# Kernel optimization log

Hardware: AMD Instinct MI355X
Metric: run time of the kernel (lower is better)

## Reference

```python
import jax, jax.numpy as jnp
import numpy as np
import math

EPS = 1e-6
NUM_HEADS = 8


def _layernorm(x, g, b):
    mu = jnp.mean(x, axis=-1, keepdims=True)
    var = jnp.mean(jnp.square(x - mu), axis=-1, keepdims=True)
    return (x - mu) * jax.lax.rsqrt(var + EPS) * g + b


def _pos_embed(n, d):
    pos = jnp.arange(n, dtype=jnp.float32)[:, None]                  # [N,1]
    div = jnp.exp(jnp.arange(0, d, 2, dtype=jnp.float32) * (-math.log(10000.0) / d))
    ang = pos * div                                                  # [N,d/2]
    pe = jnp.stack([jnp.sin(ang), jnp.cos(ang)], axis=-1).reshape(n, d)
    return pe


def setup_inputs() -> dict:
    key = jax.random.key(0)
    B, N, C, L = 2, 2048, 256, 4
    ks = jax.random.split(key, 6)
    s = 0.02
    return {
        "x": jax.random.normal(ks[0], (B, N, C), jnp.float32),
        "qkv_w": jax.random.normal(ks[1], (L, C, 3 * C), jnp.float32) * s,
        "proj_w": jax.random.normal(ks[2], (L, C, C), jnp.float32) * s,
        "proj_b": jnp.zeros((L, C), jnp.float32),
        "w1": jax.random.normal(ks[3], (L, C, C), jnp.float32) * s,
        "b1": jnp.zeros((L, C), jnp.float32),
        "w2": jax.random.normal(ks[4], (L, C, C), jnp.float32) * s,
        "b2": jnp.zeros((L, C), jnp.float32),
        "g1": jnp.ones((L, C), jnp.float32),
        "be1": jnp.zeros((L, C), jnp.float32),
        "g2": jnp.ones((L, C), jnp.float32),
        "be2": jnp.zeros((L, C), jnp.float32),
    }


def reference(x, qkv_w, proj_w, proj_b, w1, b1, w2, b2, g1, be1, g2, be2):
    B, N, C = x.shape
    L = qkv_w.shape[0]
    H = NUM_HEADS
    dh = C // H
    scale = dh ** -0.5

    x = x + _pos_embed(N, C)[None]

    for l in range(L):
        # --- attention (manual QKV, post-norm residual as in source) ---
        qkv = (x @ qkv_w[l]).reshape(B, N, 3, H, dh)
        q, k, v = qkv[:, :, 0], qkv[:, :, 1], qkv[:, :, 2]           # [B,N,H,dh]
        attn = jnp.einsum('bqhd,bkhd->bhqk', q, k) * scale           # [B,H,N,N]
        attn = jax.nn.softmax(attn, axis=-1)
        o = jnp.einsum('bhqk,bkhd->bqhd', attn, v).reshape(B, N, C)
        o = o @ proj_w[l] + proj_b[l]
        x = _layernorm(x + o, g1[l], be1[l])
        # --- MLP (GELU exact, as torch nn.GELU default) ---
        m = jax.nn.gelu(x @ w1[l] + b1[l], approximate=False) @ w2[l] + b2[l]
        x = _layernorm(x + m, g2[l], be2[l])
    return x
```

## Files before the change

kernel.cpp:

```cpp
#include <hip/hip_runtime.h>
#include <math.h>

#define Bd 2
#define Nd 2048
#define Cd 256
#define Ld 4
#define Hd 8
#define Md (Bd*Nd)
#define BHd 16
#define U32d 1024
#define SPLITd 4

typedef __attribute__((ext_vector_type(8))) short bf16x8;
typedef __attribute__((ext_vector_type(4))) float f32x4;
typedef __attribute__((ext_vector_type(16))) float f32x16;
typedef __attribute__((ext_vector_type(4))) short shortx4;

static __device__ inline f32x4 mfma16(bf16x8 a, bf16x8 b, f32x4 c) {
    return __builtin_amdgcn_mfma_f32_16x16x32_bf16(a, b, c, 0, 0, 0);
}
static __device__ inline f32x16 mfma32(bf16x8 a, bf16x8 b, f32x16 c) {
    return __builtin_amdgcn_mfma_f32_32x32x16_bf16(a, b, c, 0, 0, 0);
}
static __device__ inline short f2bf(float f) {
    union { float f; unsigned u; } v; v.f = f;
    unsigned r = (v.u + 0x7fff + ((v.u >> 16) & 1)) >> 16;
    return (short)r;
}
static __device__ inline unsigned pkbf(float a, float b) {
    unsigned r;
    asm("v_cvt_pk_bf16_f32 %0, %1, %2" : "=v"(r) : "v"(a), "v"(b));
    return r;
}
static __device__ inline float bf2f(unsigned u) {
    return __uint_as_float((u & 0xffffu) << 16);
}

__global__ __launch_bounds__(256)
void prep_kernel(const float* __restrict__ x_in, const float* __restrict__ qkv_w,
                 const float* __restrict__ proj_w, const float* __restrict__ w1,
                 const float* __restrict__ w2, float* __restrict__ xf,
                 short* __restrict__ xb, short* __restrict__ qkvT,
                 short* __restrict__ projT, short* __restrict__ w1T,
                 short* __restrict__ w2T, float qscale)
{
    __shared__ float tile[32][33];
    int id = blockIdx.x;
    if (id < 1536) {
        const float* src; short* dst; int Nc; float scale; int lim; int rem; int l;
        if (id < 768)       { l = id / 192;         rem = id % 192; src = qkv_w;  dst = qkvT;  Nc = 768; scale = qscale; lim = 256; }
        else if (id < 1024) { l = (id - 768) / 64;  rem = (id - 768) % 64;  src = proj_w; dst = projT; Nc = 256; scale = 1.f; lim = 0; }
        else if (id < 1280) { l = (id - 1024) / 64; rem = (id - 1024) % 64; src = w1;     dst = w1T;   Nc = 256; scale = 1.f; lim = 0; }
        else                { l = (id - 1280) / 64; rem = (id - 1280) % 64; src = w2;     dst = w2T;   Nc = 256; scale = 1.f; lim = 0; }
        int nb = Nc >> 5;
        int c0 = (rem % nb) * 32, k0 = (rem / nb) * 32;
        src += (size_t)l * 256 * Nc;
        dst += (size_t)l * Nc * 256;
        int tx = threadIdx.x & 31, ty = threadIdx.x >> 5;
#pragma unroll
        for (int i = 0; i < 4; i++) {
            int k = ty + 8 * i;
            tile[k][tx] = src[(size_t)(k0 + k) * Nc + c0 + tx];
        }
        __syncthreads();
#pragma unroll
        for (int i = 0; i < 4; i++) {
            int cc = ty + 8 * i;
            int col = c0 + cc;
            float v = tile[tx][cc];
            if (col < lim) v *= scale;
            dst[(size_t)col * 256 + k0 + tx] = f2bf(v);
        }
    } else {
        int i = (id - 1536) * 256 + threadIdx.x;
        int c = i & (Cd - 1);
        int n = (i >> 8) & (Nd - 1);
        const float kneg = -9.210340371976184f / 256.0f;
        float div = __expf((float)(c & ~1) * kneg);
        float ang = (float)n * div;
        float pe = (c & 1) ? cosf(ang) : sinf(ang);
        float v = x_in[i] + pe;
        xf[i] = v;
        xb[i] = f2bf(v);
    }
}

__global__ __launch_bounds__(256)
void qkv_gemm_kernel(const short* __restrict__ Ab, const short* __restrict__ WT,
                     short* __restrict__ Qh, short* __restrict__ Kh,
                     short* __restrict__ Vtb)
{
    int t = threadIdx.x, w = t >> 6, l = t & 63, c = l & 15, g = l >> 4;
    int rowBase = blockIdx.y * 128 + w * 32;
    int colBase = blockIdx.x * 32;
    const f32x4 zero = {0.f, 0.f, 0.f, 0.f};
    f32x4 acc[2][2] = {{zero, zero}, {zero, zero}};
    const short* ap0 = Ab + (size_t)(rowBase + c) * 256 + g * 8;
    const short* ap1 = ap0 + 16 * 256;
    const short* bp0 = WT + (size_t)(colBase + c) * 256 + g * 8;
    const short* bp1 = bp0 + 16 * 256;
#pragma unroll
    for (int kc = 0; kc < 256; kc += 32) {
        bf16x8 a0 = *(const bf16x8*)(ap0 + kc);
        bf16x8 a1 = *(const bf16x8*)(ap1 + kc);
        bf16x8 b0 = *(const bf16x8*)(bp0 + kc);
        bf16x8 b1 = *(const bf16x8*)(bp1 + kc);
        acc[0][0] = mfma16(a0, b0, acc[0][0]);
        acc[0][1] = mfma16(a0, b1, acc[0][1]);
        acc[1][0] = mfma16(a1, b0, acc[1][0]);
        acc[1][1] = mfma16(a1, b1, acc[1][1]);
    }
    int region = colBase >> 8;
    if (region < 2) {
        short* dst = (region == 0) ? Qh : Kh;
        int cb = colBase - region * 256;
#pragma unroll
        for (int m = 0; m < 2; m++)
#pragma unroll
            for (int n = 0; n < 2; n++) {
                int col = cb + 16 * n + c;
                int h = col >> 5, dh = col & 31;
#pragma unroll
                for (int r = 0; r < 4; r++) {
                    int tok = rowBase + 16 * m + 4 * g + r;
                    int b = tok >> 11, nt = tok & (Nd - 1);
                    dst[((size_t)(b * Hd + h) * Nd + nt) * 32 + dh] = f2bf(acc[m][n][r]);
                }
            }
    } else {
        int b = rowBase >> 11;
        int ntok0 = (rowBase & (Nd - 1)) + 4 * g;
#pragma unroll
        for (int m = 0; m < 2; m++)
#pragma unroll
            for (int n = 0; n < 2; n++) {
                int chg = colBase - 512 + 16 * n + c;
                shortx4 pkv;
#pragma unroll
                for (int r = 0; r < 4; r++) pkv[r] = f2bf(acc[m][n][r]);
                *(shortx4*)&Vtb[(size_t)((b * Hd + (chg >> 5)) * 32 + (chg & 31)) * Nd
                                + ntok0 + 16 * m] = pkv;
            }
    }
}

__global__ __launch_bounds__(256)
void attn_part_kernel(const short* __restrict__ Qh, const short* __restrict__ Kh,
                      const short* __restrict__ Vtb, unsigned* __restrict__ OPb,
                      float* __restrict__ Lsum)
{
    __shared__ short Ks[2][64 * 40];
    __shared__ short Vs[2][32 * 72];

    int t = threadIdx.x, w = t >> 6, l = t & 63;
    int l5 = l >> 5, q32 = l & 31;
    int bid = blockIdx.x;
    int xcd = bid & 7, j = bid >> 3;
    int grp = xcd * 8 + (j >> 4);
    int qt = (j & 15) * 4 + w;
    int part = grp >> 4, bh = grp & 15;

    int skey = t >> 2, sdh = (t & 3) * 8;
    int vrow = t >> 3, vcol = (t & 7) * 8;

    const int kstart = part * (Nd / SPLITd);
    const short* kg = Kh + ((size_t)bh * Nd + kstart + skey) * 32 + sdh;
    const short* vg = Vtb + ((size_t)bh * 32 + vrow) * Nd + kstart + vcol;

    bf16x8 qf0, qf1;
    {
        const short* qp = Qh + ((size_t)bh * Nd + qt * 32 + q32) * 32 + 8 * l5;
        qf0 = *(const bf16x8*)qp;
        qf1 = *(const bf16x8*)(qp + 16);
    }

    f32x16 O;
#pragma unroll
    for (int i = 0; i < 16; i++) O[i] = 0.f;
    float lsum = 0.f;

    {
        bf16x8 kr = *(const bf16x8*)kg;
        bf16x8 vr = *(const bf16x8*)vg;
        *(bf16x8*)&Ks[0][skey * 40 + sdh] = kr;
        *(bf16x8*)&Vs[0][vrow * 72 + vcol] = vr;
    }
    __syncthreads();

    const int NT = (Nd / SPLITd) / 64;
    int cur = 0;
    for (int it = 0; it < NT; ++it) {
        bool has_next = (it + 1) < NT;
        bf16x8 krn, vrn;
        if (has_next) {
            kg += 64 * 32;
            vg += 64;
            krn = *(const bf16x8*)kg;
            vrn = *(const bf16x8*)vg;
        }

        bf16x8 kf[2][2], vv[4];
#pragma unroll
        for (int sb = 0; sb < 2; sb++)
#pragma unroll
            for (int ks = 0; ks < 2; ks++)
                kf[sb][ks] = *(const bf16x8*)&Ks[cur][(32 * sb + q32) * 40 + 8 * l5 + 16 * ks];
#pragma unroll
        for (int kc = 0; kc < 4; kc++)
            vv[kc] = *(const bf16x8*)&Vs[cur][q32 * 72 + 8 * l5 + 16 * kc];

#pragma unroll
        for (int sb = 0; sb < 2; sb++) {
            f32x16 s;
#pragma unroll
            for (int i = 0; i < 16; i++) s[i] = 0.f;
            s = mfma32(kf[sb][0], qf0, s);
            s = mfma32(kf[sb][1], qf1, s);
            float e[16];
#pragma unroll
            for (int i = 0; i < 16; i++) e[i] = exp2f(s[i]);
            float p0 = e[0] + e[1],  p1 = e[2] + e[3];
            float p2 = e[4] + e[5],  p3 = e[6] + e[7];
            float p4 = e[8] + e[9],  p5 = e[10] + e[11];
            float p6 = e[12] + e[13], p7 = e[14] + e[15];
            p0 += p1; p2 += p3; p4 += p5; p6 += p7;
            p0 += p2; p4 += p6;
            lsum += p0 + p4;
            unsigned wd[8];
#pragma unroll
            for (int i = 0; i < 8; i++) wd[i] = pkbf(e[2 * i], e[2 * i + 1]);
#pragma unroll
            for (int half = 0; half < 2; half++) {
                unsigned a0 = wd[4 * half], a1 = wd[4 * half + 1];
                unsigned b0 = wd[4 * half + 2], b1 = wd[4 * half + 3];
                asm("v_permlane32_swap_b32 %0, %1" : "+v"(a0), "+v"(b0));
                asm("v_permlane32_swap_b32 %0, %1" : "+v"(a1), "+v"(b1));
                union { unsigned u[4]; bf16x8 v; } pa;
                pa.u[0] = a0; pa.u[1] = a1; pa.u[2] = b0; pa.u[3] = b1;
                O = mfma32(pa.v, vv[2 * sb + half], O);
            }
        }

        if (has_next) {
            *(bf16x8*)&Ks[cur ^ 1][skey * 40 + sdh] = krn;
            *(bf16x8*)&Vs[cur ^ 1][vrow * 72 + vcol] = vrn;
            __syncthreads();
            cur ^= 1;
        }
    }

    lsum += __shfl_xor(lsum, 32, 64);

    int u = bh * 64 + qt;
    unsigned* opb = OPb + ((size_t)part * U32d + u) * 512;
#pragma unroll
    for (int i = 0; i < 16; i += 2) {
        int q = (i & 3) + 8 * (i >> 2) + 4 * l5;
        opb[(q >> 1) * 32 + q32] = pkbf(O[i], O[i + 1]);
    }
    if (l5 == 0) Lsum[((size_t)part * U32d + u) * 32 + q32] = lsum;
}

__global__ __launch_bounds__(512)
void proj_ln_kernel(const unsigned* __restrict__ OPb, const float* __restrict__ Lsum,
                    const short* __restrict__ WT, const float* __restrict__ bias,
                    const float* __restrict__ resid, const float* __restrict__ gg,
                    const float* __restrict__ be, float* __restrict__ outf,
                    short* __restrict__ outb)
{
    __shared__ short Atile[16 * 264];
    __shared__ float red[8][16][2];
    int t = threadIdx.x;
    int rowBase = blockIdx.x * 16;

    {
        int r = t >> 5, seg = t & 31;
        int grow = rowBase + r;
        int bb = grow >> 11;
        int qt = (grow & (Nd - 1)) >> 5;
        int q = grow & 31;
        int h = seg >> 2;
        int dh0 = (seg & 3) * 8;
        int u = (bb * Hd + h) * 64 + qt;
        int sh = (q & 1) * 16;
        float o[8] = {0.f, 0.f, 0.f, 0.f, 0.f, 0.f, 0.f, 0.f};
        float L = 0.f;
#pragma unroll
        for (int p = 0; p < SPLITd; p++) {
            const unsigned* src = OPb + ((size_t)p * U32d + u) * 512 + (q >> 1) * 32 + dh0;
            uint4 w0 = *(const uint4*)src;
            uint4 w1 = *(const uint4*)(src + 4);
            o[0] += bf2f(w0.x >> sh); o[1] += bf2f(w0.y >> sh);
            o[2] += bf2f(w0.z >> sh); o[3] += bf2f(w0.w >> sh);
            o[4] += bf2f(w1.x >> sh); o[5] += bf2f(w1.y >> sh);
            o[6] += bf2f(w1.z >> sh); o[7] += bf2f(w1.w >> sh);
            L += Lsum[((size_t)p * U32d + u) * 32 + q];
        }
        float inv = 1.f / L;
        bf16x8 pk;
#pragma unroll
        for (int j = 0; j < 8; j++) pk[j] = f2bf(o[j] * inv);
        *(bf16x8*)&Atile[r * 264 + seg * 8] = pk;
    }
    __syncthreads();

    int w = t >> 6, l = t & 63, c = l & 15, g = l >> 4;
    const f32x4 zero = {0.f, 0.f, 0.f, 0.f};
    f32x4 acc0 = zero, acc1 = zero;
    const short* bp0 = WT + (size_t)(w * 32 + c) * 256 + g * 8;
    const short* bp1 = bp0 + 16 * 256;
#pragma unroll
    for (int kc = 0; kc < 256; kc += 32) {
        bf16x8 a = *(const bf16x8*)&Atile[c * 264 + g * 8 + kc];
        acc0 = mfma16(a, *(const bf16x8*)(bp0 + kc), acc0);
        acc1 = mfma16(a, *(const bf16x8*)(bp1 + kc), acc1);
    }

    float vv[2][4], s_[4] = {0.f, 0.f, 0.f, 0.f}, sq_[4] = {0.f, 0.f, 0.f, 0.f};
    int col0 = w * 32 + c, col1 = col0 + 16;
    float bi0 = bias[col0], bi1 = bias[col1];
#pragma unroll
    for (int r = 0; r < 4; r++) {
        int row = rowBase + 4 * g + r;
        float v0 = acc0[r] + bi0 + resid[(size_t)row * 256 + col0];
        float v1 = acc1[r] + bi1 + resid[(size_t)row * 256 + col1];
        vv[0][r] = v0; vv[1][r] = v1;
        s_[r] += v0 + v1; sq_[r] += v0 * v0 + v1 * v1;
    }
#pragma unroll
    for (int off = 1; off <= 8; off <<= 1)
#pragma unroll
        for (int r = 0; r < 4; r++) {
            s_[r] += __shfl_xor(s_[r], off, 64);
            sq_[r] += __shfl_xor(sq_[r], off, 64);
        }
    if (c == 0)
#pragma unroll
        for (int r = 0; r < 4; r++) {
            red[w][4 * g + r][0] = s_[r];
            red[w][4 * g + r][1] = sq_[r];
        }
    __syncthreads();
    float mu[4], rs[4];
#pragma unroll
    for (int r = 0; r < 4; r++) {
        float S = 0.f, Q = 0.f;
#pragma unroll
        for (int ww = 0; ww < 8; ww++) { S += red[ww][4 * g + r][0]; Q += red[ww][4 * g + r][1]; }
        mu[r] = S * (1.f / 256.f);
        rs[r] = rsqrtf(Q * (1.f / 256.f) - mu[r] * mu[r] + 1e-6f);
    }
    float gv0 = gg[col0], bv0 = be[col0], gv1 = gg[col1], bv1 = be[col1];
#pragma unroll
    for (int r = 0; r < 4; r++) {
        int row = rowBase + 4 * g + r;
        float o0 = (vv[0][r] - mu[r]) * rs[r] * gv0 + bv0;
        float o1 = (vv[1][r] - mu[r]) * rs[r] * gv1 + bv1;
        outf[(size_t)row * 256 + col0] = o0;
        outf[(size_t)row * 256 + col1] = o1;
        outb[(size_t)row * 256 + col0] = f2bf(o0);
        outb[(size_t)row * 256 + col1] = f2bf(o1);
    }
}

template<int LAST>
__global__ __launch_bounds__(512)
void mlp_kernel(const short* __restrict__ xbin, const short* __restrict__ W1T,
                const float* __restrict__ b1, const short* __restrict__ W2T,
                const float* __restrict__ b2, const float* __restrict__ resid,
                const float* __restrict__ gg, const float* __restrict__ be,
                float* __restrict__ outf, short* __restrict__ outb)
{
    __shared__ short A1[16 * 264];
    __shared__ short A2[16 * 264];
    __shared__ float red[8][16][2];
    int t = threadIdx.x;
    int rowBase = blockIdx.x * 16;

    {
        int r = t >> 5, seg = t & 31;
        *(bf16x8*)&A1[r * 264 + seg * 8] =
            *(const bf16x8*)(xbin + (size_t)(rowBase + r) * 256 + seg * 8);
    }
    __syncthreads();

    int w = t >> 6, l = t & 63, c = l & 15, g = l >> 4;
    const f32x4 zero = {0.f, 0.f, 0.f, 0.f};
    int col0 = w * 32 + c, col1 = col0 + 16;

    {
        f32x4 acc0 = zero, acc1 = zero;
        const short* bp0 = W1T + (size_t)(w * 32 + c) * 256 + g * 8;
        const short* bp1 = bp0 + 16 * 256;
#pragma unroll
        for (int kc = 0; kc < 256; kc += 32) {
            bf16x8 a = *(const bf16x8*)&A1[c * 264 + g * 8 + kc];
            acc0 = mfma16(a, *(const bf16x8*)(bp0 + kc), acc0);
            acc1 = mfma16(a, *(const bf16x8*)(bp1 + kc), acc1);
        }
        float bi0 = b1[col0], bi1 = b1[col1];
#pragma unroll
        for (int r = 0; r < 4; r++) {
            float v0 = acc0[r] + bi0, v1 = acc1[r] + bi1;
            v0 = 0.5f * v0 * (1.f + erff(v0 * 0.7071067811865476f));
            v1 = 0.5f * v1 * (1.f + erff(v1 * 0.7071067811865476f));
            A2[(4 * g + r) * 264 + col0] = f2bf(v0);
            A2[(4 * g + r) * 264 + col1] = f2bf(v1);
        }
    }
    __syncthreads();

    f32x4 acc0 = zero, acc1 = zero;
    const short* bp0 = W2T + (size_t)(w * 32 + c) * 256 + g * 8;
    const short* bp1 = bp0 + 16 * 256;
#pragma unroll
    for (int kc = 0; kc < 256; kc += 32) {
        bf16x8 a = *(const bf16x8*)&A2[c * 264 + g * 8 + kc];
        acc0 = mfma16(a, *(const bf16x8*)(bp0 + kc), acc0);
        acc1 = mfma16(a, *(const bf16x8*)(bp1 + kc), acc1);
    }
    float vv[2][4], s_[4] = {0.f, 0.f, 0.f, 0.f}, sq_[4] = {0.f, 0.f, 0.f, 0.f};
    float bi0 = b2[col0], bi1 = b2[col1];
#pragma unroll
    for (int r = 0; r < 4; r++) {
        int row = rowBase + 4 * g + r;
        float v0 = acc0[r] + bi0 + resid[(size_t)row * 256 + col0];
        float v1 = acc1[r] + bi1 + resid[(size_t)row * 256 + col1];
        vv[0][r] = v0; vv[1][r] = v1;
        s_[r] += v0 + v1; sq_[r] += v0 * v0 + v1 * v1;
    }
#pragma unroll
    for (int off = 1; off <= 8; off <<= 1)
#pragma unroll
        for (int r = 0; r < 4; r++) {
            s_[r] += __shfl_xor(s_[r], off, 64);
            sq_[r] += __shfl_xor(sq_[r], off, 64);
        }
    if (c == 0)
#pragma unroll
        for (int r = 0; r < 4; r++) {
            red[w][4 * g + r][0] = s_[r];
            red[w][4 * g + r][1] = sq_[r];
        }
    __syncthreads();
    float mu[4], rs[4];
#pragma unroll
    for (int r = 0; r < 4; r++) {
        float S = 0.f, Q = 0.f;
#pragma unroll
        for (int ww = 0; ww < 8; ww++) { S += red[ww][4 * g + r][0]; Q += red[ww][4 * g + r][1]; }
        mu[r] = S * (1.f / 256.f);
        rs[r] = rsqrtf(Q * (1.f / 256.f) - mu[r] * mu[r] + 1e-6f);
    }
    float gv0 = gg[col0], bv0 = be[col0], gv1 = gg[col1], bv1 = be[col1];
#pragma unroll
    for (int r = 0; r < 4; r++) {
        int row = rowBase + 4 * g + r;
        float o0 = (vv[0][r] - mu[r]) * rs[r] * gv0 + bv0;
        float o1 = (vv[1][r] - mu[r]) * rs[r] * gv1 + bv1;
        outf[(size_t)row * 256 + col0] = o0;
        outf[(size_t)row * 256 + col1] = o1;
        if (!LAST) {
            outb[(size_t)row * 256 + col0] = f2bf(o0);
            outb[(size_t)row * 256 + col1] = f2bf(o1);
        }
    }
}

extern "C" void kernel_launch(void* const* d_in, const int* in_sizes, int n_in,
                              void* d_out, int out_size, void* d_ws, size_t ws_size,
                              hipStream_t stream)
{
    const float* x_in   = (const float*)d_in[0];
    const float* qkv_w  = (const float*)d_in[1];
    const float* proj_w = (const float*)d_in[2];
    const float* proj_b = (const float*)d_in[3];
    const float* w1     = (const float*)d_in[4];
    const float* b1     = (const float*)d_in[5];
    const float* w2     = (const float*)d_in[6];
    const float* b2     = (const float*)d_in[7];
    const float* g1     = (const float*)d_in[8];
    const float* be1    = (const float*)d_in[9];
    const float* g2     = (const float*)d_in[10];
    const float* be2    = (const float*)d_in[11];
    float* outp = (float*)d_out;

    char* p = (char*)d_ws;
    float* xf    = (float*)p;    p += (size_t)Md * Cd * 4;
    short* xb    = (short*)p;    p += (size_t)Md * Cd * 2;
    short* Qh    = (short*)p;    p += (size_t)Md * Cd * 2;
    short* Kh    = (short*)p;    p += (size_t)Md * Cd * 2;
    short* Vtb   = (short*)p;    p += (size_t)Md * Cd * 2;
    unsigned* OPb = (unsigned*)p; p += (size_t)SPLITd * U32d * 512 * 4;
    float* Lsum  = (float*)p;    p += (size_t)SPLITd * U32d * 32 * 4;
    short* qkvT  = (short*)p;    p += (size_t)Ld * 768 * 256 * 2;
    short* projT = (short*)p;    p += (size_t)Ld * 256 * 256 * 2;
    short* w1T   = (short*)p;    p += (size_t)Ld * 256 * 256 * 2;
    short* w2T   = (short*)p;    p += (size_t)Ld * 256 * 256 * 2;

    const float QSCALE = 0.17677669529663687f * 1.4426950408889634f;
    prep_kernel<<<1536 + Md * Cd / 256, 256, 0, stream>>>(
        x_in, qkv_w, proj_w, w1, w2, xf, xb, qkvT, projT, w1T, w2T, QSCALE);

    for (int l = 0; l < Ld; l++) {
        qkv_gemm_kernel<<<dim3(24, 32), 256, 0, stream>>>(
            xb, qkvT + (size_t)l * 768 * 256, Qh, Kh, Vtb);
        attn_part_kernel<<<1024, 256, 0, stream>>>(Qh, Kh, Vtb, OPb, Lsum);
        proj_ln_kernel<<<Md / 16, 512, 0, stream>>>(
            OPb, Lsum, projT + (size_t)l * 65536, proj_b + l * 256, xf,
            g1 + l * 256, be1 + l * 256, xf, xb);
        if (l == Ld - 1)
            mlp_kernel<1><<<Md / 16, 512, 0, stream>>>(
                xb, w1T + (size_t)l * 65536, b1 + l * 256,
                w2T + (size_t)l * 65536, b2 + l * 256, xf,
                g2 + l * 256, be2 + l * 256, outp, nullptr);
        else
            mlp_kernel<0><<<Md / 16, 512, 0, stream>>>(
                xb, w1T + (size_t)l * 65536, b1 + l * 256,
                w2T + (size_t)l * 65536, b2 + l * 256, xf,
                g2 + l * 256, be2 + l * 256, xf, xb);
    }
}
```

Measured before the change: 323.2 us.

## Fuse projection+LayerNorm with MLP into one tail kernel; widen attention blocks

Merges the attention output projection, first LayerNorm, both MLP GEMMs with GELU and the second LayerNorm into one tail kernel per layer. The LN1 result stays in registers and LDS instead of being written to and re-read from global memory, and one launch per layer is removed. The attention kernel is also reworked to 512 threads (8 waves, 8 q-tiles per block). Half the threads now load the K tile and half the V tile, so each thread issues one global load per step instead of two. The cost is higher LDS use in the tail kernel and a different occupancy pattern for attention.

Result: faster. 301.5 us (-6.7%).

```diff
diff --git a/kernel.cpp b/kernel.cpp
--- a/kernel.cpp
+++ b/kernel.cpp
@@ -144,7 +144,7 @@
     }
 }
 
-__global__ __launch_bounds__(256)
+__global__ __launch_bounds__(512)
 void attn_part_kernel(const short* __restrict__ Qh, const short* __restrict__ Kh,
                       const short* __restrict__ Vtb, unsigned* __restrict__ OPb,
                       float* __restrict__ Lsum)
@@ -156,16 +156,21 @@
     int l5 = l >> 5, q32 = l & 31;
     int bid = blockIdx.x;
     int xcd = bid & 7, j = bid >> 3;
-    int grp = xcd * 8 + (j >> 4);
-    int qt = (j & 15) * 4 + w;
+    int grp = xcd * 8 + (j >> 3);
+    int qt = (j & 7) * 8 + w;
     int part = grp >> 4, bh = grp & 15;
 
-    int skey = t >> 2, sdh = (t & 3) * 8;
-    int vrow = t >> 3, vcol = (t & 7) * 8;
+    bool isK = (t < 256);
+    int t2 = t & 255;
+    int koff = (t2 >> 2) * 40 + (t2 & 3) * 8;
+    int voff = (t2 >> 3) * 72 + (t2 & 7) * 8;
+    int soff = isK ? koff : voff;
+    long sstep = isK ? 64 * 32 : 64;
 
     const int kstart = part * (Nd / SPLITd);
-    const short* kg = Kh + ((size_t)bh * Nd + kstart + skey) * 32 + sdh;
-    const short* vg = Vtb + ((size_t)bh * 32 + vrow) * Nd + kstart + vcol;
+    const short* sg = isK
+        ? Kh + ((size_t)bh * Nd + kstart + (t2 >> 2)) * 32 + (t2 & 3) * 8
+        : Vtb + ((size_t)bh * 32 + (t2 >> 3)) * Nd + kstart + (t2 & 7) * 8;
 
     bf16x8 qf0, qf1;
     {
@@ -180,10 +185,8 @@
     float lsum = 0.f;
 
     {
-        bf16x8 kr = *(const bf16x8*)kg;
-        bf16x8 vr = *(const bf16x8*)vg;
-        *(bf16x8*)&Ks[0][skey * 40 + sdh] = kr;
-        *(bf16x8*)&Vs[0][vrow * 72 + vcol] = vr;
+        bf16x8 r0 = *(const bf16x8*)sg;
+        *(bf16x8*)((isK ? Ks[0] : Vs[0]) + soff) = r0;
     }
     __syncthreads();
 
@@ -191,12 +194,10 @@
     int cur = 0;
     for (int it = 0; it < NT; ++it) {
         bool has_next = (it + 1) < NT;
-        bf16x8 krn, vrn;
+        bf16x8 nxt;
         if (has_next) {
-            kg += 64 * 32;
-            vg += 64;
-            krn = *(const bf16x8*)kg;
-            vrn = *(const bf16x8*)vg;
+            sg += sstep;
+            nxt = *(const bf16x8*)sg;
         }
 
         bf16x8 kf[2][2], vv[4];
@@ -242,8 +243,7 @@
         }
 
         if (has_next) {
-            *(bf16x8*)&Ks[cur ^ 1][skey * 40 + sdh] = krn;
-            *(bf16x8*)&Vs[cur ^ 1][vrow * 72 + vcol] = vrn;
+            *(bf16x8*)((isK ? Ks[cur ^ 1] : Vs[cur ^ 1]) + soff) = nxt;
             __syncthreads();
             cur ^= 1;
         }
@@ -261,14 +261,20 @@
     if (l5 == 0) Lsum[((size_t)part * U32d + u) * 32 + q32] = lsum;
 }
 
+template<int LAST>
 __global__ __launch_bounds__(512)
-void proj_ln_kernel(const unsigned* __restrict__ OPb, const float* __restrict__ Lsum,
-                    const short* __restrict__ WT, const float* __restrict__ bias,
-                    const float* __restrict__ resid, const float* __restrict__ gg,
-                    const float* __restrict__ be, float* __restrict__ outf,
-                    short* __restrict__ outb)
+void tail_kernel(const unsigned* __restrict__ OPb, const float* __restrict__ Lsum,
+                 const short* __restrict__ WT, const float* __restrict__ bias,
+                 const float* __restrict__ resid,
+                 const float* __restrict__ g1v, const float* __restrict__ be1v,
+                 const short* __restrict__ W1T, const float* __restrict__ b1v,
+                 const short* __restrict__ W2T, const float* __restrict__ b2v,
+                 const float* __restrict__ g2v, const float* __restrict__ be2v,
+                 float* __restrict__ outf, short* __restrict__ outb)
 {
     __shared__ short Atile[16 * 264];
+    __shared__ short A1[16 * 264];
+    __shared__ short A2[16 * 264];
     __shared__ float red[8][16][2];
     int t = threadIdx.x;
     int rowBase = blockIdx.x * 16;
@@ -306,26 +312,31 @@
 
     int w = t >> 6, l = t & 63, c = l & 15, g = l >> 4;
     const f32x4 zero = {0.f, 0.f, 0.f, 0.f};
+    int col0 = w * 32 + c, col1 = col0 + 16;
+
     f32x4 acc0 = zero, acc1 = zero;
-    const short* bp0 = WT + (size_t)(w * 32 + c) * 256 + g * 8;
-    const short* bp1 = bp0 + 16 * 256;
-#pragma unroll
-    for (int kc = 0; kc < 256; kc += 32) {
-        bf16x8 a = *(const bf16x8*)&Atile[c * 264 + g * 8 + kc];
-        acc0 = mfma16(a, *(const bf16x8*)(bp0 + kc), acc0);
-        acc1 = mfma16(a, *(const bf16x8*)(bp1 + kc), acc1);
+    {
+        const short* bp0 = WT + (size_t)col0 * 256 + g * 8;
+        const short* bp1 = WT + (size_t)col1 * 256 + g * 8;
+#pragma unroll
+        for (int kc = 0; kc < 256; kc += 32) {
+            bf16x8 a = *(const bf16x8*)&Atile[c * 264 + g * 8 + kc];
+            acc0 = mfma16(a, *(const bf16x8*)(bp0 + kc), acc0);
+            acc1 = mfma16(a, *(const bf16x8*)(bp1 + kc), acc1);
+        }
     }
 
     float vv[2][4], s_[4] = {0.f, 0.f, 0.f, 0.f}, sq_[4] = {0.f, 0.f, 0.f, 0.f};
-    int col0 = w * 32 + c, col1 = col0 + 16;
-    float bi0 = bias[col0], bi1 = bias[col1];
-#pragma unroll
-    for (int r = 0; r < 4; r++) {
-        int row = rowBase + 4 * g + r;
-        float v0 = acc0[r] + bi0 + resid[(size_t)row * 256 + col0];
-        float v1 = acc1[r] + bi1 + resid[(size_t)row * 256 + col1];
-        vv[0][r] = v0; vv[1][r] = v1;
-        s_[r] += v0 + v1; sq_[r] += v0 * v0 + v1 * v1;
+    {
+        float bi0 = bias[col0], bi1 = bias[col1];
+#pragma unroll
+        for (int r = 0; r < 4; r++) {
+            int row = rowBase + 4 * g + r;
+            float v0 = acc0[r] + bi0 + resid[(size_t)row * 256 + col0];
+            float v1 = acc1[r] + bi1 + resid[(size_t)row * 256 + col1];
+            vv[0][r] = v0; vv[1][r] = v1;
+            s_[r] += v0 + v1; sq_[r] += v0 * v0 + v1 * v1;
+        }
     }
 #pragma unroll
     for (int off = 1; off <= 8; off <<= 1)
@@ -341,67 +352,43 @@
             red[w][4 * g + r][1] = sq_[r];
         }
     __syncthreads();
-    float mu[4], rs[4];
-#pragma unroll
-    for (int r = 0; r < 4; r++) {
-        float S = 0.f, Q = 0.f;
-#pragma unroll
-        for (int ww = 0; ww < 8; ww++) { S += red[ww][4 * g + r][0]; Q += red[ww][4 * g + r][1]; }
-        mu[r] = S * (1.f / 256.f);
-        rs[r] = rsqrtf(Q * (1.f / 256.f) - mu[r] * mu[r] + 1e-6f);
-    }
-    float gv0 = gg[col0], bv0 = be[col0], gv1 = gg[col1], bv1 = be[col1];
-#pragma unroll
-    for (int r = 0; r < 4; r++) {
-        int row = rowBase + 4 * g + r;
-        float o0 = (vv[0][r] - mu[r]) * rs[r] * gv0 + bv0;
-        float o1 = (vv[1][r] - mu[r]) * rs[r] * gv1 + bv1;
-        outf[(size_t)row * 256 + col0] = o0;
-        outf[(size_t)row * 256 + col1] = o1;
-        outb[(size_t)row * 256 + col0] = f2bf(o0);
-        outb[(size_t)row * 256 + col1] = f2bf(o1);
-    }
-}
-
-template<int LAST>
-__global__ __launch_bounds__(512)
-void mlp_kernel(const short* __restrict__ xbin, const short* __restrict__ W1T,
-                const float* __restrict__ b1, const short* __restrict__ W2T,
-                const float* __restrict__ b2, const float* __restrict__ resid,
-                const float* __restrict__ gg, const float* __restrict__ be,
-                float* __restrict__ outf, short* __restrict__ outb)
-{
-    __shared__ short A1[16 * 264];
-    __shared__ short A2[16 * 264];
-    __shared__ float red[8][16][2];
-    int t = threadIdx.x;
-    int rowBase = blockIdx.x * 16;
-
-    {
-        int r = t >> 5, seg = t & 31;
-        *(bf16x8*)&A1[r * 264 + seg * 8] =
-            *(const bf16x8*)(xbin + (size_t)(rowBase + r) * 256 + seg * 8);
+    float ln1[2][4];
+    {
+        float mu[4], rs[4];
+#pragma unroll
+        for (int r = 0; r < 4; r++) {
+            float S = 0.f, Q = 0.f;
+#pragma unroll
+            for (int ww = 0; ww < 8; ww++) { S += red[ww][4 * g + r][0]; Q += red[ww][4 * g + r][1]; }
+            mu[r] = S * (1.f / 256.f);
+            rs[r] = rsqrtf(Q * (1.f / 256.f) - mu[r] * mu[r] + 1e-6f);
+        }
+        float gv0 = g1v[col0], bv0 = be1v[col0], gv1 = g1v[col1], bv1 = be1v[col1];
+#pragma unroll
+        for (int r = 0; r < 4; r++) {
+            float o0 = (vv[0][r] - mu[r]) * rs[r] * gv0 + bv0;
+            float o1 = (vv[1][r] - mu[r]) * rs[r] * gv1 + bv1;
+            ln1[0][r] = o0; ln1[1][r] = o1;
+            A1[(4 * g + r) * 264 + col0] = f2bf(o0);
+            A1[(4 * g + r) * 264 + col1] = f2bf(o1);
+        }
     }
     __syncthreads();
 
-    int w = t >> 6, l = t & 63, c = l & 15, g = l >> 4;
-    const f32x4 zero = {0.f, 0.f, 0.f, 0.f};
-    int col0 = w * 32 + c, col1 = col0 + 16;
-
-    {
-        f32x4 acc0 = zero, acc1 = zero;
-        const short* bp0 = W1T + (size_t)(w * 32 + c) * 256 + g * 8;
-        const short* bp1 = bp0 + 16 * 256;
+    {
+        f32x4 a0 = zero, a1 = zero;
+        const short* bp0 = W1T + (size_t)col0 * 256 + g * 8;
+        const short* bp1 = W1T + (size_t)col1 * 256 + g * 8;
 #pragma unroll
         for (int kc = 0; kc < 256; kc += 32) {
             bf16x8 a = *(const bf16x8*)&A1[c * 264 + g * 8 + kc];
-            acc0 = mfma16(a, *(const bf16x8*)(bp0 + kc), acc0);
-            acc1 = mfma16(a, *(const bf16x8*)(bp1 + kc), acc1);
-        }
-        float bi0 = b1[col0], bi1 = b1[col1];
-#pragma unroll
-        for (int r = 0; r < 4; r++) {
-            float v0 = acc0[r] + bi0, v1 = acc1[r] + bi1;
+            a0 = mfma16(a, *(const bf16x8*)(bp0 + kc), a0);
+            a1 = mfma16(a, *(const bf16x8*)(bp1 + kc), a1);
+        }
+        float bi0 = b1v[col0], bi1 = b1v[col1];
+#pragma unroll
+        for (int r = 0; r < 4; r++) {
+            float v0 = a0[r] + bi0, v1 = a1[r] + bi1;
             v0 = 0.5f * v0 * (1.f + erff(v0 * 0.7071067811865476f));
             v1 = 0.5f * v1 * (1.f + erff(v1 * 0.7071067811865476f));
             A2[(4 * g + r) * 264 + col0] = f2bf(v0);
@@ -410,59 +397,64 @@
     }
     __syncthreads();
 
-    f32x4 acc0 = zero, acc1 = zero;
-    const short* bp0 = W2T + (size_t)(w * 32 + c) * 256 + g * 8;
-    const short* bp1 = bp0 + 16 * 256;
-#pragma unroll
-    for (int kc = 0; kc < 256; kc += 32) {
-        bf16x8 a = *(const bf16x8*)&A2[c * 264 + g * 8 + kc];
-        acc0 = mfma16(a, *(const bf16x8*)(bp0 + kc), acc0);
-        acc1 = mfma16(a, *(const bf16x8*)(bp1 + kc), acc1);
-    }
-    float vv[2][4], s_[4] = {0.f, 0.f, 0.f, 0.f}, sq_[4] = {0.f, 0.f, 0.f, 0.f};
-    float bi0 = b2[col0], bi1 = b2[col1];
-#pragma unroll
-    for (int r = 0; r < 4; r++) {
-        int row = rowBase + 4 * g + r;
-        float v0 = acc0[r] + bi0 + resid[(size_t)row * 256 + col0];
-        float v1 = acc1[r] + bi1 + resid[(size_t)row * 256 + col1];
-        vv[0][r] = v0; vv[1][r] = v1;
-        s_[r] += v0 + v1; sq_[r] += v0 * v0 + v1 * v1;
-    }
-#pragma unroll
-    for (int off = 1; off <= 8; off <<= 1)
-#pragma unroll
-        for (int r = 0; r < 4; r++) {
-            s_[r] += __shfl_xor(s_[r], off, 64);
-            sq_[r] += __shfl_xor(sq_[r], off, 64);
-        }
-    if (c == 0)
-#pragma unroll
-        for (int r = 0; r < 4; r++) {
-            red[w][4 * g + r][0] = s_[r];
-            red[w][4 * g + r][1] = sq_[r];
-        }
+    acc0 = zero; acc1 = zero;
+    {
+        const short* bp0 = W2T + (size_t)col0 * 256 + g * 8;
+        const short* bp1 = W2T + (size_t)col1 * 256 + g * 8;
+#pragma unroll
+        for (int kc = 0; kc < 256; kc += 32) {
+            bf16x8 a = *(const bf16x8*)&A2[c * 264 + g * 8 + kc];
+            acc0 = mfma16(a, *(const bf16x8*)(bp0 + kc), acc0);
+            acc1 = mfma16(a, *(const bf16x8*)(bp1 + kc), acc1);
+        }
+    }
+    {
+        float bi0 = b2v[col0], bi1 = b2v[col1];
+        float t0[4] = {0.f, 0.f, 0.f, 0.f}, t1[4] = {0.f, 0.f, 0.f, 0.f};
+#pragma unroll
+        for (int r = 0; r < 4; r++) {
+            float v0 = acc0[r] + bi0 + ln1[0][r];
+            float v1 = acc1[r] + bi1 + ln1[1][r];
+            vv[0][r] = v0; vv[1][r] = v1;
+            t0[r] = v0 + v1; t1[r] = v0 * v0 + v1 * v1;
+        }
+#pragma unroll
+        for (int off = 1; off <= 8; off <<= 1)
+#pragma unroll
+            for (int r = 0; r < 4; r++) {
+                t0[r] += __shfl_xor(t0[r], off, 64);
+                t1[r] += __shfl_xor(t1[r], off, 64);
+            }
+        if (c == 0)
+#pragma unroll
+            for (int r = 0; r < 4; r++) {
+                red[w][4 * g + r][0] = t0[r];
+                red[w][4 * g + r][1] = t1[r];
+            }
+    }
     __syncthreads();
-    float mu[4], rs[4];
-#pragma unroll
-    for (int r = 0; r < 4; r++) {
-        float S = 0.f, Q = 0.f;
-#pragma unroll
-        for (int ww = 0; ww < 8; ww++) { S += red[ww][4 * g + r][0]; Q += red[ww][4 * g + r][1]; }
-        mu[r] = S * (1.f / 256.f);
-        rs[r] = rsqrtf(Q * (1.f / 256.f) - mu[r] * mu[r] + 1e-6f);
-    }
-    float gv0 = gg[col0], bv0 = be[col0], gv1 = gg[col1], bv1 = be[col1];
-#pragma unroll
-    for (int r = 0; r < 4; r++) {
-        int row = rowBase + 4 * g + r;
-        float o0 = (vv[0][r] - mu[r]) * rs[r] * gv0 + bv0;
-        float o1 = (vv[1][r] - mu[r]) * rs[r] * gv1 + bv1;
-        outf[(size_t)row * 256 + col0] = o0;
-        outf[(size_t)row * 256 + col1] = o1;
-        if (!LAST) {
-            outb[(size_t)row * 256 + col0] = f2bf(o0);
-            outb[(size_t)row * 256 + col1] = f2bf(o1);
+    {
+        float mu[4], rs[4];
+#pragma unroll
+        for (int r = 0; r < 4; r++) {
+            float S = 0.f, Q = 0.f;
+#pragma unroll
+            for (int ww = 0; ww < 8; ww++) { S += red[ww][4 * g + r][0]; Q += red[ww][4 * g + r][1]; }
+            mu[r] = S * (1.f / 256.f);
+            rs[r] = rsqrtf(Q * (1.f / 256.f) - mu[r] * mu[r] + 1e-6f);
+        }
+        float gv0 = g2v[col0], bv0 = be2v[col0], gv1 = g2v[col1], bv1 = be2v[col1];
+#pragma unroll
+        for (int r = 0; r < 4; r++) {
+            int row = rowBase + 4 * g + r;
+            float o0 = (vv[0][r] - mu[r]) * rs[r] * gv0 + bv0;
+            float o1 = (vv[1][r] - mu[r]) * rs[r] * gv1 + bv1;
+            outf[(size_t)row * 256 + col0] = o0;
+            outf[(size_t)row * 256 + col1] = o1;
+            if (!LAST) {
+                outb[(size_t)row * 256 + col0] = f2bf(o0);
+                outb[(size_t)row * 256 + col1] = f2bf(o1);
+            }
         }
     }
 }
@@ -505,19 +497,20 @@
     for (int l = 0; l < Ld; l++) {
         qkv_gemm_kernel<<<dim3(24, 32), 256, 0, stream>>>(
             xb, qkvT + (size_t)l * 768 * 256, Qh, Kh, Vtb);
-        attn_part_kernel<<<1024, 256, 0, stream>>>(Qh, Kh, Vtb, OPb, Lsum);
-        proj_ln_kernel<<<Md / 16, 512, 0, stream>>>(
-            OPb, Lsum, projT + (size_t)l * 65536, proj_b + l * 256, xf,
-            g1 + l * 256, be1 + l * 256, xf, xb);
+        attn_part_kernel<<<512, 512, 0, stream>>>(Qh, Kh, Vtb, OPb, Lsum);
         if (l == Ld - 1)
-            mlp_kernel<1><<<Md / 16, 512, 0, stream>>>(
-                xb, w1T + (size_t)l * 65536, b1 + l * 256,
-                w2T + (size_t)l * 65536, b2 + l * 256, xf,
+            tail_kernel<1><<<Md / 16, 512, 0, stream>>>(
+                OPb, Lsum, projT + (size_t)l * 65536, proj_b + l * 256, xf,
+                g1 + l * 256, be1 + l * 256,
+                w1T + (size_t)l * 65536, b1 + l * 256,
+                w2T + (size_t)l * 65536, b2 + l * 256,
                 g2 + l * 256, be2 + l * 256, outp, nullptr);
         else
-            mlp_kernel<0><<<Md / 16, 512, 0, stream>>>(
-                xb, w1T + (size_t)l * 65536, b1 + l * 256,
-                w2T + (size_t)l * 65536, b2 + l * 256, xf,
+            tail_kernel<0><<<Md / 16, 512, 0, stream>>>(
+                OPb, Lsum, projT + (size_t)l * 65536, proj_b + l * 256, xf,
+                g1 + l * 256, be1 + l * 256,
+                w1T + (size_t)l * 65536, b1 + l * 256,
+                w2T + (size_t)l * 65536, b2 + l * 256,
                 g2 + l * 256, be2 + l * 256, xf, xb);
     }
 }
```
